# Performance work log

Hardware: AMD Instinct MI355X
Metric: run time of the kernel (lower is better)

The kernel has to match this reference:

```python
import jax, jax.numpy as jnp
import numpy as np

SQRT_2_OVER_PI = 0.79788456

def gelu_tanh(x):
    # tanh-approximate GELU, matches torch F.gelu(approximate='tanh')
    return 0.5 * x * (1.0 + jnp.tanh(SQRT_2_OVER_PI * x * (1.0 + 0.044715 * x * x)))

def gelu_bwd(x):
    # analytical derivative of tanh-approx GELU (same constants as source)
    t = jnp.tanh(SQRT_2_OVER_PI * x * (1.0 + 0.044715 * x * x))
    return 0.5 * x * ((1.0 - t * t) * (SQRT_2_OVER_PI + 0.1070322243 * x * x)) + 0.5 * (1.0 + t)

def setup_inputs() -> dict:
    key = jax.random.key(0)
    ks = jax.random.split(key, 6)
    T, d_phi, d_h = 8192, 4096, 64
    d_mid = 4 * d_h
    return {
        "phi_seq": jax.random.normal(ks[0], (T, d_phi), jnp.float32),
        "C_seq": jax.random.uniform(ks[1], (T,), jnp.float32),
        "theta_K_w": jax.random.normal(ks[2], (d_h, d_phi), jnp.float32) * 0.02,
        "theta_Q_w": jax.random.normal(ks[3], (d_h, d_phi), jnp.float32) * 0.02,
        "W10": jax.random.normal(ks[4], (d_h, d_mid), jnp.float32) * 0.02,
        "b10": jnp.zeros((d_mid,), jnp.float32),
        "W20": jax.random.normal(ks[5], (d_mid,), jnp.float32) * 0.02,
        "b20": jnp.zeros((), jnp.float32),
        "log_eta": jnp.asarray(np.log(0.01), jnp.float32),
    }

def reference(phi_seq, C_seq, theta_K_w, theta_Q_w, W10, b10, W20, b20, log_eta):
    eta = jnp.exp(log_eta)
    # Slow-weight projections hoisted out of the scan (same math, one big GEMM)
    u_Q = phi_seq @ theta_Q_w.T  # [T, d_h]
    u_K = phi_seq @ theta_K_w.T  # [T, d_h]

    def step(carry, inp):
        W1, b1, W2, b2 = carry
        u_q, u_k = inp
        # score with current fast weights
        s = jax.nn.sigmoid(gelu_tanh(u_q @ W1 + b1) @ W2 + b2)
        # update fast weights (inner objective, C_t = 0.0)
        Z1 = u_k @ W1 + b1          # [d_mid]
        X2 = gelu_tanh(Z1)
        pred = jax.nn.sigmoid(X2 @ W2 + b2)
        d_Z2 = 2.0 * pred * pred * (1.0 - pred)  # d/dZ2 of (pred-0)^2
        d_Z1 = (d_Z2 * W2) * gelu_bwd(Z1)
        new_carry = (
            W1 - eta * jnp.outer(u_k, d_Z1),
            b1 - eta * d_Z1,
            W2 - eta * d_Z2 * X2,
            b2 - eta * d_Z2,
        )
        return new_carry, s

    _, scores = jax.lax.scan(step, (W10, b10, W20, b20), (u_Q, u_K))
    outer_loss = jnp.sum((scores - C_seq) ** 2)
    return scores, outer_loss
```

## Files before the change

kernel.cpp:

```cpp
#include <hip/hip_runtime.h>
#include <hip/hip_bf16.h>

#define DH 64
#define DM 256

typedef float f32x2 __attribute__((ext_vector_type(2)));

__device__ __forceinline__ f32x2 sp2(float s) { return (f32x2){s, s}; }
__device__ __forceinline__ f32x2 pkfma(f32x2 a, f32x2 b, f32x2 c) {
#if __has_builtin(__builtin_elementwise_fma)
    return __builtin_elementwise_fma(a, b, c);
#else
    f32x2 r; r.x = fmaf(a.x, b.x, c.x); r.y = fmaf(a.y, b.y, c.y); return r;
#endif
}

__device__ __forceinline__ float tanh_fast(float y) {
    float e = __expf(2.0f * y);
    return 1.0f - 2.0f / (e + 1.0f);
}
__device__ __forceinline__ float sigmoid_fast(float x) {
    return 1.0f / (1.0f + __expf(-x));
}

template <int CTRL, int RMASK>
__device__ __forceinline__ float dpp_term(float x) {
    int p = __builtin_amdgcn_update_dpp(0, __float_as_int(x), CTRL, RMASK, 0xf, false);
    return __int_as_float(p);
}
__device__ __forceinline__ float wave_sum63(float x) {
    x += dpp_term<0xB1,  0xf>(x);
    x += dpp_term<0x4E,  0xf>(x);
    x += dpp_term<0x141, 0xf>(x);
    x += dpp_term<0x140, 0xf>(x);
    x += dpp_term<0x142, 0xa>(x);
    x += dpp_term<0x143, 0xc>(x);
    return x;
}

__global__ __launch_bounds__(256) void proj_kernel(
    const float* __restrict__ phi,
    const float* __restrict__ thK,
    const float* __restrict__ thQ,
    float* __restrict__ u,
    int dphi)
{
    const int tid  = threadIdx.x;
    const int th32 = tid & 31;
    const int tt8  = tid >> 5;
    const int t0   = tt8 * 4;
    const int h0   = th32 * 4;
    const int T0   = blockIdx.x * 32;

    __shared__ float sPhiT[32][36];
    __shared__ float sThT[32][128];

    const int h   = tid >> 1;
    const int ko  = (tid & 1) * 16;
    const float* trow = (h < 64) ? (thQ + (size_t)h * dphi)
                                 : (thK + (size_t)(h - 64) * dphi);
    const int tr  = tid >> 3;
    const int k4p = (tid & 7) * 4;

    float4 pv, tv0, tv1, tv2, tv3;
    pv  = *(const float4*)&phi[(size_t)(T0 + tr) * dphi + k4p];
    tv0 = *(const float4*)&trow[ko + 0];
    tv1 = *(const float4*)&trow[ko + 4];
    tv2 = *(const float4*)&trow[ko + 8];
    tv3 = *(const float4*)&trow[ko + 12];

    float acc[4][4];
    #pragma unroll
    for (int i = 0; i < 4; ++i)
        #pragma unroll
        for (int jj = 0; jj < 4; ++jj) acc[i][jj] = 0.0f;

    const int NC = dphi / 32;
    for (int c = 0; c < NC; ++c) {
        __syncthreads();
        sPhiT[k4p + 0][tr] = pv.x;
        sPhiT[k4p + 1][tr] = pv.y;
        sPhiT[k4p + 2][tr] = pv.z;
        sPhiT[k4p + 3][tr] = pv.w;
        sThT[ko +  0][h] = tv0.x;  sThT[ko +  1][h] = tv0.y;
        sThT[ko +  2][h] = tv0.z;  sThT[ko +  3][h] = tv0.w;
        sThT[ko +  4][h] = tv1.x;  sThT[ko +  5][h] = tv1.y;
        sThT[ko +  6][h] = tv1.z;  sThT[ko +  7][h] = tv1.w;
        sThT[ko +  8][h] = tv2.x;  sThT[ko +  9][h] = tv2.y;
        sThT[ko + 10][h] = tv2.z;  sThT[ko + 11][h] = tv2.w;
        sThT[ko + 12][h] = tv3.x;  sThT[ko + 13][h] = tv3.y;
        sThT[ko + 14][h] = tv3.z;  sThT[ko + 15][h] = tv3.w;
        __syncthreads();
        if (c + 1 < NC) {
            const int kb = (c + 1) * 32;
            pv  = *(const float4*)&phi[(size_t)(T0 + tr) * dphi + kb + k4p];
            tv0 = *(const float4*)&trow[kb + ko + 0];
            tv1 = *(const float4*)&trow[kb + ko + 4];
            tv2 = *(const float4*)&trow[kb + ko + 8];
            tv3 = *(const float4*)&trow[kb + ko + 12];
        }
        #pragma unroll 8
        for (int k = 0; k < 32; ++k) {
            float4 ph = *(const float4*)&sPhiT[k][t0];
            float4 th = *(const float4*)&sThT[k][h0];
            acc[0][0] = fmaf(ph.x, th.x, acc[0][0]);
            acc[0][1] = fmaf(ph.x, th.y, acc[0][1]);
            acc[0][2] = fmaf(ph.x, th.z, acc[0][2]);
            acc[0][3] = fmaf(ph.x, th.w, acc[0][3]);
            acc[1][0] = fmaf(ph.y, th.x, acc[1][0]);
            acc[1][1] = fmaf(ph.y, th.y, acc[1][1]);
            acc[1][2] = fmaf(ph.y, th.z, acc[1][2]);
            acc[1][3] = fmaf(ph.y, th.w, acc[1][3]);
            acc[2][0] = fmaf(ph.z, th.x, acc[2][0]);
            acc[2][1] = fmaf(ph.z, th.y, acc[2][1]);
            acc[2][2] = fmaf(ph.z, th.z, acc[2][2]);
            acc[2][3] = fmaf(ph.z, th.w, acc[2][3]);
            acc[3][0] = fmaf(ph.w, th.x, acc[3][0]);
            acc[3][1] = fmaf(ph.w, th.y, acc[3][1]);
            acc[3][2] = fmaf(ph.w, th.z, acc[3][2]);
            acc[3][3] = fmaf(ph.w, th.w, acc[3][3]);
        }
    }
    #pragma unroll
    for (int i = 0; i < 4; ++i) {
        float4 o;
        o.x = acc[i][0]; o.y = acc[i][1]; o.z = acc[i][2]; o.w = acc[i][3];
        *(float4*)&u[(size_t)(T0 + t0 + i) * 128 + h0] = o;
    }
}

__global__ __launch_bounds__(256) void dots2_kernel(
    const float* __restrict__ u, float2* __restrict__ dd2, int T)
{
    const int t    = (blockIdx.x * 256 + threadIdx.x) >> 6;
    const int lane = threadIdx.x & 63;
    if (t >= T) return;
    float ukt = u[(size_t)t * 128 + 64 + lane];
    float k1 = (t >= 1) ? u[(size_t)(t - 1) * 128 + 64 + lane] : 0.f;
    float k2 = (t >= 2) ? u[(size_t)(t - 2) * 128 + 64 + lane] : 0.f;
    float p1 = k1 * ukt, p2 = k2 * ukt;
    #pragma unroll
    for (int off = 32; off > 0; off >>= 1) {
        p1 += __shfl_xor(p1, off);
        p2 += __shfl_xor(p2, off);
    }
    if (lane == 0) dd2[t] = make_float2(p1, p2);
}

__global__ __launch_bounds__(256, 1) void scan_k4(
    const float* __restrict__ u,
    const float2* __restrict__ dd2g,
    const float* __restrict__ W10,
    const float* __restrict__ b10,
    const float* __restrict__ W20,
    const float* __restrict__ b20,
    const float* __restrict__ log_eta,
    float* __restrict__ e1s,
    float* __restrict__ g2s,
    float* __restrict__ dz2s,
    int T)
{
    const int j    = threadIdx.x;
    const int lane = j & 63;
    const int wv   = j >> 6;
    const int uko  = 16 * wv;

    __shared__ __align__(16) float  ubuf[2][64][68];
    __shared__ __align__(16) float  pbuf[2][4][256];
    __shared__ __align__(16) float  ebufT[4][4][72];
    __shared__ __align__(16) float  pqk[2][4];
    __shared__ __align__(16) float2 dbuf[2][64];

    const int NB = T >> 6;
    const int sl = j >> 2, qq = j & 3;

    {
        const float* src = u + (size_t)sl * 128 + 64 + qq * 16;
        #pragma unroll
        for (int k = 0; k < 4; ++k)
            *(float4*)&ubuf[0][sl][qq * 16 + k * 4] = *(const float4*)&src[k * 4];
        if (j < 64) dbuf[0][j] = dd2g[j];
        if (j < 4)  pqk[1][j] = -2.5e29f;
        float* ez = &ebufT[2][0][0];
        for (int k = j; k < 2 * 4 * 72; k += 256) ez[k] = 0.f;
    }

    f32x2 w1p[32];
    #pragma unroll
    for (int i = 0; i < 16; ++i) {
        float4 wr = *(const float4*)&W10[(uko + i) * DM + lane * 4];
        w1p[2 * i]     = (f32x2){wr.x, wr.y};
        w1p[2 * i + 1] = (f32x2){wr.z, wr.w};
    }
    float b1j = b10[j];
    float w2j = W20[j];
    float b2  = b20[0];
    const float eta = __expf(log_eta[0]);
    float dZ2p = 0.f, en1 = 0.f, en2 = 0.f, x2p = 0.f;

    __syncthreads();

    {
        const float* ur0 = &ubuf[0][0][uko];
        f32x2 a0 = sp2(0.f), a1 = sp2(0.f);
        #pragma unroll
        for (int q = 0; q < 4; ++q) {
            float4 us = *(const float4*)&ur0[q * 4];
            a0 = pkfma(sp2(us.x), w1p[8*q+0], a0); a1 = pkfma(sp2(us.x), w1p[8*q+1], a1);
            a0 = pkfma(sp2(us.y), w1p[8*q+2], a0); a1 = pkfma(sp2(us.y), w1p[8*q+3], a1);
            a0 = pkfma(sp2(us.z), w1p[8*q+4], a0); a1 = pkfma(sp2(us.z), w1p[8*q+5], a1);
            a0 = pkfma(sp2(us.w), w1p[8*q+6], a0); a1 = pkfma(sp2(us.w), w1p[8*q+7], a1);
        }
        float4 wk; wk.x = a0.x; wk.y = a0.y; wk.z = a1.x; wk.w = a1.y;
        *(float4*)&pbuf[0][wv][lane * 4] = wk;
    }
    __syncthreads();

    float4 st[4];
    float2 std2 = make_float2(0.f, 0.f);

    for (int t = 0; t < T; ++t) {
        const int r   = t & 63;
        const int B   = t >> 6;
        const int bs  = B & 1;
        const int pbR = t & 1;

        float4 pqK = *(const float4*)&pqk[pbR ^ 1][0];
        const int sE = (t + 2) & 3;
        float eb0 = ebufT[sE][0][lane];
        float eb1 = ebufT[sE][1][lane];
        float eb2 = ebufT[sE][2][lane];
        float eb3 = ebufT[sE][3][lane];
        float2 dd = dbuf[bs][r];
        float pB0 = pbuf[pbR][0][j], pB1 = pbuf[pbR][1][j];
        float pB2 = pbuf[pbR][2][j], pB3 = pbuf[pbR][3][j];
        const int rn = (t + 1 < T) ? t + 1 : T - 1;
        const int rm = (t >= 2) ? t - 2 : 0;
        const float* urN = &ubuf[(rn >> 6) & 1][rn & 63][uko];
        const float* urM = &ubuf[(rm >> 6) & 1][rm & 63][uko];
        float4 n0 = *(const float4*)&urN[0],  n1 = *(const float4*)&urN[4];
        float4 n2 = *(const float4*)&urN[8],  n3 = *(const float4*)&urN[12];
        float4 m0 = *(const float4*)&urM[0],  m1 = *(const float4*)&urM[4];
        float4 m2 = *(const float4*)&urM[8],  m3 = *(const float4*)&urM[12];

        float zp   = ((pqK.x + pqK.y) + (pqK.z + pqK.w)) + b2;
        float pred = sigmoid_fast(zp);
        float dZ2  = 2.f * pred * pred * (1.f - pred);
        float e1o  = dZ2 * en1;
        if (t > 0) {
            e1s[(size_t)(t - 1) * 256 + j] = e1o;
            g2s[(size_t)(t - 1) * 256 + j] = dZ2 * x2p;
            if (j == 0) dz2s[t - 1] = dZ2;
        }

        f32x2 e1g0 = sp2(dZ2p) * (f32x2){eb0, eb1};
        f32x2 e1g1 = sp2(dZ2p) * (f32x2){eb2, eb3};
        f32x2 a0 = sp2(0.f), a1 = sp2(0.f);
#define ROWK(ib, ums, uns) {                                   \
        f32x2 wa = pkfma(sp2(-(ums)), e1g0, w1p[ib]);          \
        f32x2 wb = pkfma(sp2(-(ums)), e1g1, w1p[(ib) + 1]);    \
        w1p[ib] = wa; w1p[(ib) + 1] = wb;                      \
        a0 = pkfma(sp2(uns), wa, a0);                          \
        a1 = pkfma(sp2(uns), wb, a1); }
        ROWK(0,  m0.x, n0.x); ROWK(2,  m0.y, n0.y);
        ROWK(4,  m0.z, n0.z); ROWK(6,  m0.w, n0.w);
        ROWK(8,  m1.x, n1.x); ROWK(10, m1.y, n1.y);
        ROWK(12, m1.z, n1.z); ROWK(14, m1.w, n1.w);
        ROWK(16, m2.x, n2.x); ROWK(18, m2.y, n2.y);
        ROWK(20, m2.z, n2.z); ROWK(22, m2.w, n2.w);
        ROWK(24, m3.x, n3.x); ROWK(26, m3.y, n3.y);
        ROWK(28, m3.z, n3.z); ROWK(30, m3.w, n3.w);
#undef ROWK
        { float4 wk; wk.x = a0.x; wk.y = a0.y; wk.z = a1.x; wk.w = a1.y;
          *(float4*)&pbuf[pbR ^ 1][wv][lane * 4] = wk; }

        float e1o2 = dZ2p * en2;
        b1j -= e1o;
        w2j  = fmaf(-eta * dZ2, x2p, w2j);
        b2  -= eta * dZ2;
        float Pk = ((pB0 + pB1) + (pB2 + pB3));
        float zk = Pk + b1j - e1o2 * dd.y - e1o * dd.x;
        float tk = tanh_fast(0.79788456f * zk * fmaf(0.044715f, zk * zk, 1.f));
        float x2 = 0.5f * zk * (1.f + tk);
        float gb = 0.5f * zk * ((1.f - tk * tk) *
                   fmaf(0.1070322243f, zk * zk, 0.79788456f))
                 + 0.5f * (1.f + tk);
        float en = eta * w2j * gb;
        ebufT[t & 3][j & 3][j >> 2] = en;
        float pk = wave_sum63(x2 * w2j);
        if (lane == 63) pqk[t & 1][wv] = pk;

        dZ2p = dZ2; en2 = en1; en1 = en; x2p = x2;

        if (r == 0 && B + 1 < NB) {
            const float* src = u + (size_t)((B + 1) * 64 + sl) * 128 + 64 + qq * 16;
            #pragma unroll
            for (int k = 0; k < 4; ++k) st[k] = *(const float4*)&src[k * 4];
            if (j < 64) std2 = dd2g[(B + 1) * 64 + j];
        }
        if (r == 32 && B + 1 < NB) {
            #pragma unroll
            for (int k = 0; k < 4; ++k)
                *(float4*)&ubuf[bs ^ 1][sl][qq * 16 + k * 4] = st[k];
            if (j < 64) dbuf[bs ^ 1][j] = std2;
        }

        asm volatile("s_waitcnt lgkmcnt(0)" ::: "memory");
        __builtin_amdgcn_s_barrier();
        asm volatile("" ::: "memory");
    }

    {
        float4 pqK = *(const float4*)&pqk[(T - 1) & 1][0];
        float zp   = ((pqK.x + pqK.y) + (pqK.z + pqK.w)) + b2;
        float pred = sigmoid_fast(zp);
        float dZ2  = 2.f * pred * pred * (1.f - pred);
        e1s[(size_t)(T - 1) * 256 + j] = dZ2 * en1;
        g2s[(size_t)(T - 1) * 256 + j] = dZ2 * x2p;
        if (j == 0) dz2s[T - 1] = dZ2;
    }
}

#define TB 32
__global__ __launch_bounds__(256) void scores_kernel(
    const float* __restrict__ u,
    const float* __restrict__ e1s,
    const float* __restrict__ g2s,
    const float* __restrict__ dz2s,
    const float* __restrict__ W10,
    const float* __restrict__ b10,
    const float* __restrict__ W20,
    const float* __restrict__ b20,
    const float* __restrict__ log_eta,
    float* __restrict__ out,
    int T)
{
    const int tid = threadIdx.x;
    const int t0  = blockIdx.x * TB;
    const int j   = tid;
    const int wv  = tid >> 6;
    const int lane = tid & 63;

    __shared__ __align__(16) float uq[TB][68];
    __shared__ __align__(16) float uk[TB][68];
    __shared__ __align__(16) float Dl[TB][36];
    __shared__ float redl[2][4];

    #pragma unroll
    for (int k = 0; k < 2; ++k) {
        int idx = tid * 2 + k;
        int tl = idx >> 4, c4 = idx & 15;
        *(float4*)&uq[tl][c4 * 4] = *(const float4*)&u[(size_t)(t0 + tl) * 128 + c4 * 4];
    }
    const float eta = __expf(log_eta[0]);
    float w2p = W20[j];
    float b2p = b20[0];
    float b1j = b10[j];
    __syncthreads();

    float acc[TB];
    {
        float wcol[64];
        #pragma unroll
        for (int i = 0; i < 64; ++i) wcol[i] = W10[i * DM + j];
        for (int tl = 0; tl < TB; ++tl) {
            float a = b1j;
            #pragma unroll
            for (int q = 0; q < 16; ++q) {
                float4 uv = *(const float4*)&uq[tl][q * 4];
                a = fmaf(uv.x, wcol[4*q+0], a);
                a = fmaf(uv.y, wcol[4*q+1], a);
                a = fmaf(uv.z, wcol[4*q+2], a);
                a = fmaf(uv.w, wcol[4*q+3], a);
            }
            acc[tl] = a;
        }
    }

    const int nchunk = t0 / TB + 1;
    for (int c = 0; c < nchunk; ++c) {
        const int sc = c * TB;
        __syncthreads();
        #pragma unroll
        for (int k = 0; k < 2; ++k) {
            int idx = tid * 2 + k;
            int sl = idx >> 4, c4 = idx & 15;
            *(float4*)&uk[sl][c4 * 4] = *(const float4*)&u[(size_t)(sc + sl) * 128 + 64 + c4 * 4];
        }
        __syncthreads();
        {
            int tl = tid & 31, sg = tid >> 5;
            float4 uqr[16];
            #pragma unroll
            for (int q = 0; q < 16; ++q) uqr[q] = *(const float4*)&uq[tl][q * 4];
            #pragma unroll
            for (int k = 0; k < 4; ++k) {
                int sl = sg * 4 + k;
                float d = 0.f;
                #pragma unroll
                for (int q = 0; q < 16; ++q) {
                    float4 ukr = *(const float4*)&uk[sl][q * 4];
                    d = fmaf(ukr.x, uqr[q].x, d);
                    d = fmaf(ukr.y, uqr[q].y, d);
                    d = fmaf(ukr.z, uqr[q].z, d);
                    d = fmaf(ukr.w, uqr[q].w, d);
                }
                Dl[sl][tl] = d;
            }
        }
        __syncthreads();

        const bool lastc = (c == nchunk - 1);
        if (!lastc) {
            float e1acc = 0.f;
            for (int sl = 0; sl < TB; ++sl) {
                const int s = sc + sl;
                float e1v = e1s[(size_t)s * 256 + j];
                float g2v = g2s[(size_t)s * 256 + j];
                float dzv = dz2s[s];
                w2p = fmaf(-eta, g2v, w2p);
                b2p = fmaf(-eta, dzv, b2p);
                e1acc += e1v;
                float4 dreg[8];
                #pragma unroll
                for (int q = 0; q < 8; ++q) dreg[q] = *(const float4*)&Dl[sl][q * 4];
                #pragma unroll
                for (int tl = 0; tl < TB; ++tl) {
                    float D = (tl & 2) ? ((tl & 1) ? dreg[tl>>2].w : dreg[tl>>2].z)
                                       : ((tl & 1) ? dreg[tl>>2].y : dreg[tl>>2].x);
                    acc[tl] = fmaf(-e1v, D, acc[tl]);
                }
            }
            #pragma unroll
            for (int tl = 0; tl < TB; ++tl) acc[tl] -= e1acc;
        } else {
            for (int sl = 0; sl < TB; ++sl) {
                const int s = sc + sl;
                float zq = 0.f;
                #pragma unroll
                for (int tl = 0; tl < TB; ++tl) if (tl == sl) zq = acc[tl];
                float tq = tanh_fast(0.79788456f * zq * fmaf(0.044715f, zq*zq, 1.f));
                float aq = 0.5f * zq * (1.f + tq);
                float v  = wave_sum63(aq * w2p);
                if (lane == 63) redl[sl & 1][wv] = v;
                __syncthreads();
                float zs = redl[sl & 1][0] + redl[sl & 1][1] + redl[sl & 1][2] + redl[sl & 1][3] + b2p;
                if (tid == 0) out[t0 + sl] = sigmoid_fast(zs);

                float e1v = e1s[(size_t)s * 256 + j];
                float g2v = g2s[(size_t)s * 256 + j];
                float dzv = dz2s[s];
                w2p = fmaf(-eta, g2v, w2p);
                b2p = fmaf(-eta, dzv, b2p);
                float4 dreg[8];
                #pragma unroll
                for (int q = 0; q < 8; ++q) dreg[q] = *(const float4*)&Dl[sl][q * 4];
                #pragma unroll
                for (int tl = 0; tl < TB; ++tl) {
                    float D = (tl & 2) ? ((tl & 1) ? dreg[tl>>2].w : dreg[tl>>2].z)
                                       : ((tl & 1) ? dreg[tl>>2].y : dreg[tl>>2].x);
                    float e1m = (tl > sl) ? e1v : 0.f;
                    acc[tl] = fmaf(-e1m, D + 1.f, acc[tl]);
                }
            }
        }
    }
}

__global__ __launch_bounds__(256) void loss_kernel(
    const float* __restrict__ C, float* __restrict__ out, int T)
{
    const int tid = threadIdx.x;
    const int wv = tid >> 6, lane = tid & 63;
    __shared__ float part[4];
    float acc = 0.f;
    for (int t = tid; t < T; t += 256) {
        float d = out[t] - C[t];
        acc = fmaf(d, d, acc);
    }
    acc = wave_sum63(acc);
    if (lane == 63) part[wv] = acc;
    __syncthreads();
    if (tid == 0) out[T] = ((part[0] + part[1]) + (part[2] + part[3]));
}

extern "C" void kernel_launch(void* const* d_in, const int* in_sizes, int n_in,
                              void* d_out, int out_size, void* d_ws, size_t ws_size,
                              hipStream_t stream) {
    const float* phi     = (const float*)d_in[0];
    const float* C_seq   = (const float*)d_in[1];
    const float* thK     = (const float*)d_in[2];
    const float* thQ     = (const float*)d_in[3];
    const float* W10     = (const float*)d_in[4];
    const float* b10     = (const float*)d_in[5];
    const float* W20     = (const float*)d_in[6];
    const float* b20     = (const float*)d_in[7];
    const float* log_eta = (const float*)d_in[8];

    const int T    = in_sizes[1];
    const int dphi = in_sizes[0] / T;

    char* ws = (char*)d_ws;
    float*  uw   = (float*)(ws);
    float2* dd2  = (float2*)(ws + (size_t)T * 128 * 4);
    float*  dz2s = (float*)(ws + (size_t)T * 130 * 4);
    float*  e1s  = (float*)(ws + (size_t)T * 131 * 4);
    float*  g2s  = (float*)(ws + (size_t)T * 387 * 4);

    proj_kernel<<<T / 32, 256, 0, stream>>>(phi, thK, thQ, uw, dphi);
    dots2_kernel<<<T / 4, 256, 0, stream>>>(uw, dd2, T);
    scan_k4<<<1, 256, 0, stream>>>(uw, dd2, W10, b10, W20, b20, log_eta,
                                   e1s, g2s, dz2s, T);
    scores_kernel<<<T / TB, 256, 0, stream>>>(uw, e1s, g2s, dz2s,
                                              W10, b10, W20, b20, log_eta,
                                              (float*)d_out, T);
    loss_kernel<<<1, 256, 0, stream>>>(C_seq, (float*)d_out, T);
}
```

Before: 6.788 ms.

## Replicate per-column nonlinear work in every wave to drop cross-wave LDS exchanges

Each wave now computes the GELU, derivative and score reduction for all 256 mid columns (4 per lane) itself. It no longer has each thread handle one column and exchange the results through the ebufT and pqk shared buffers. This removes one LDS round-trip for the en values and the partial-score gather, and the score is broadcast with a readlane. The cost is four times more transcendental and ALU work per thread on the serial critical path. Global stores of e1s and g2s are vectorized and done only by wave 0.

```diff
diff --git a/kernel.cpp b/kernel.cpp
--- a/kernel.cpp
+++ b/kernel.cpp
@@ -164,11 +164,10 @@
     const int lane = j & 63;
     const int wv   = j >> 6;
     const int uko  = 16 * wv;
+    const int c0   = 4 * lane;
 
     __shared__ __align__(16) float  ubuf[2][64][68];
     __shared__ __align__(16) float  pbuf[2][4][256];
-    __shared__ __align__(16) float  ebufT[4][4][72];
-    __shared__ __align__(16) float  pqk[2][4];
     __shared__ __align__(16) float2 dbuf[2][64];
 
     const int NB = T >> 6;
@@ -180,23 +179,27 @@
         for (int k = 0; k < 4; ++k)
             *(float4*)&ubuf[0][sl][qq * 16 + k * 4] = *(const float4*)&src[k * 4];
         if (j < 64) dbuf[0][j] = dd2g[j];
-        if (j < 4)  pqk[1][j] = -2.5e29f;
-        float* ez = &ebufT[2][0][0];
-        for (int k = j; k < 2 * 4 * 72; k += 256) ez[k] = 0.f;
     }
 
     f32x2 w1p[32];
     #pragma unroll
     for (int i = 0; i < 16; ++i) {
-        float4 wr = *(const float4*)&W10[(uko + i) * DM + lane * 4];
+        float4 wr = *(const float4*)&W10[(uko + i) * DM + c0];
         w1p[2 * i]     = (f32x2){wr.x, wr.y};
         w1p[2 * i + 1] = (f32x2){wr.z, wr.w};
     }
-    float b1j = b10[j];
-    float w2j = W20[j];
+    float4 b14 = *(const float4*)&b10[c0];
+    f32x2 b1v0 = (f32x2){b14.x, b14.y}, b1v1 = (f32x2){b14.z, b14.w};
+    float4 w24 = *(const float4*)&W20[c0];
+    f32x2 w2v0 = (f32x2){w24.x, w24.y}, w2v1 = (f32x2){w24.z, w24.w};
     float b2  = b20[0];
     const float eta = __expf(log_eta[0]);
-    float dZ2p = 0.f, en1 = 0.f, en2 = 0.f, x2p = 0.f;
+
+    float dZ2p = 0.f;
+    f32x2 en1a = sp2(0.f), en1b = sp2(0.f);
+    f32x2 en2a = sp2(0.f), en2b = sp2(0.f);
+    f32x2 x2pa = sp2(0.f), x2pb = sp2(0.f);
+    float zp_prev = -2.5e29f;
 
     __syncthreads();
 
@@ -212,7 +215,7 @@
             a0 = pkfma(sp2(us.w), w1p[8*q+6], a0); a1 = pkfma(sp2(us.w), w1p[8*q+7], a1);
         }
         float4 wk; wk.x = a0.x; wk.y = a0.y; wk.z = a1.x; wk.w = a1.y;
-        *(float4*)&pbuf[0][wv][lane * 4] = wk;
+        *(float4*)&pbuf[0][wv][c0] = wk;
     }
     __syncthreads();
 
@@ -220,20 +223,16 @@
     float2 std2 = make_float2(0.f, 0.f);
 
     for (int t = 0; t < T; ++t) {
-        const int r   = t & 63;
-        const int B   = t >> 6;
-        const int bs  = B & 1;
-        const int pbR = t & 1;
-
-        float4 pqK = *(const float4*)&pqk[pbR ^ 1][0];
-        const int sE = (t + 2) & 3;
-        float eb0 = ebufT[sE][0][lane];
-        float eb1 = ebufT[sE][1][lane];
-        float eb2 = ebufT[sE][2][lane];
-        float eb3 = ebufT[sE][3][lane];
+        const int r  = t & 63;
+        const int B  = t >> 6;
+        const int bs = B & 1;
+        const int pb = t & 1;
+
+        float4 P0 = *(const float4*)&pbuf[pb][0][c0];
+        float4 P1 = *(const float4*)&pbuf[pb][1][c0];
+        float4 P2 = *(const float4*)&pbuf[pb][2][c0];
+        float4 P3 = *(const float4*)&pbuf[pb][3][c0];
         float2 dd = dbuf[bs][r];
-        float pB0 = pbuf[pbR][0][j], pB1 = pbuf[pbR][1][j];
-        float pB2 = pbuf[pbR][2][j], pB3 = pbuf[pbR][3][j];
         const int rn = (t + 1 < T) ? t + 1 : T - 1;
         const int rm = (t >= 2) ? t - 2 : 0;
         const float* urN = &ubuf[(rn >> 6) & 1][rn & 63][uko];
@@ -243,22 +242,29 @@
         float4 m0 = *(const float4*)&urM[0],  m1 = *(const float4*)&urM[4];
         float4 m2 = *(const float4*)&urM[8],  m3 = *(const float4*)&urM[12];
 
-        float zp   = ((pqK.x + pqK.y) + (pqK.z + pqK.w)) + b2;
-        float pred = sigmoid_fast(zp);
+        float pred = sigmoid_fast(zp_prev);
         float dZ2  = 2.f * pred * pred * (1.f - pred);
-        float e1o  = dZ2 * en1;
-        if (t > 0) {
-            e1s[(size_t)(t - 1) * 256 + j] = e1o;
-            g2s[(size_t)(t - 1) * 256 + j] = dZ2 * x2p;
+        f32x2 e1oa  = sp2(dZ2)  * en1a,  e1ob  = sp2(dZ2)  * en1b;
+        f32x2 e1o2a = sp2(dZ2p) * en2a,  e1o2b = sp2(dZ2p) * en2b;
+
+        if (t > 0 && wv == 0) {
+            float4 e1st; e1st.x = e1oa.x; e1st.y = e1oa.y; e1st.z = e1ob.x; e1st.w = e1ob.y;
+            *(float4*)&e1s[(size_t)(t - 1) * 256 + c0] = e1st;
+            f32x2 g2a = sp2(dZ2) * x2pa, g2b = sp2(dZ2) * x2pb;
+            float4 g2st; g2st.x = g2a.x; g2st.y = g2a.y; g2st.z = g2b.x; g2st.w = g2b.y;
+            *(float4*)&g2s[(size_t)(t - 1) * 256 + c0] = g2st;
             if (j == 0) dz2s[t - 1] = dZ2;
         }
 
-        f32x2 e1g0 = sp2(dZ2p) * (f32x2){eb0, eb1};
-        f32x2 e1g1 = sp2(dZ2p) * (f32x2){eb2, eb3};
+        b1v0 = b1v0 - e1oa;  b1v1 = b1v1 - e1ob;
+        w2v0 = pkfma(sp2(-eta * dZ2), x2pa, w2v0);
+        w2v1 = pkfma(sp2(-eta * dZ2), x2pb, w2v1);
+        b2  -= eta * dZ2;
+
         f32x2 a0 = sp2(0.f), a1 = sp2(0.f);
 #define ROWK(ib, ums, uns) {                                   \
-        f32x2 wa = pkfma(sp2(-(ums)), e1g0, w1p[ib]);          \
-        f32x2 wb = pkfma(sp2(-(ums)), e1g1, w1p[(ib) + 1]);    \
+        f32x2 wa = pkfma(sp2(-(ums)), e1o2a, w1p[ib]);         \
+        f32x2 wb = pkfma(sp2(-(ums)), e1o2b, w1p[(ib) + 1]);   \
         w1p[ib] = wa; w1p[(ib) + 1] = wb;                      \
         a0 = pkfma(sp2(uns), wa, a0);                          \
         a1 = pkfma(sp2(uns), wb, a1); }
@@ -272,25 +278,38 @@
         ROWK(28, m3.z, n3.z); ROWK(30, m3.w, n3.w);
 #undef ROWK
         { float4 wk; wk.x = a0.x; wk.y = a0.y; wk.z = a1.x; wk.w = a1.y;
-          *(float4*)&pbuf[pbR ^ 1][wv][lane * 4] = wk; }
-
-        float e1o2 = dZ2p * en2;
-        b1j -= e1o;
-        w2j  = fmaf(-eta * dZ2, x2p, w2j);
-        b2  -= eta * dZ2;
-        float Pk = ((pB0 + pB1) + (pB2 + pB3));
-        float zk = Pk + b1j - e1o2 * dd.y - e1o * dd.x;
-        float tk = tanh_fast(0.79788456f * zk * fmaf(0.044715f, zk * zk, 1.f));
-        float x2 = 0.5f * zk * (1.f + tk);
-        float gb = 0.5f * zk * ((1.f - tk * tk) *
-                   fmaf(0.1070322243f, zk * zk, 0.79788456f))
-                 + 0.5f * (1.f + tk);
-        float en = eta * w2j * gb;
-        ebufT[t & 3][j & 3][j >> 2] = en;
-        float pk = wave_sum63(x2 * w2j);
-        if (lane == 63) pqk[t & 1][wv] = pk;
-
-        dZ2p = dZ2; en2 = en1; en1 = en; x2p = x2;
+          *(float4*)&pbuf[pb ^ 1][wv][c0] = wk; }
+
+        f32x2 zka = (f32x2){(P0.x + P1.x) + (P2.x + P3.x),
+                            (P0.y + P1.y) + (P2.y + P3.y)};
+        f32x2 zkb = (f32x2){(P0.z + P1.z) + (P2.z + P3.z),
+                            (P0.w + P1.w) + (P2.w + P3.w)};
+        zka = zka + b1v0 - sp2(dd.y) * e1o2a - sp2(dd.x) * e1oa;
+        zkb = zkb + b1v1 - sp2(dd.y) * e1o2b - sp2(dd.x) * e1ob;
+
+        float z0 = zka.x, z1 = zka.y, z2 = zkb.x, z3 = zkb.y;
+        float tk0 = tanh_fast(0.79788456f * z0 * fmaf(0.044715f, z0*z0, 1.f));
+        float tk1 = tanh_fast(0.79788456f * z1 * fmaf(0.044715f, z1*z1, 1.f));
+        float tk2 = tanh_fast(0.79788456f * z2 * fmaf(0.044715f, z2*z2, 1.f));
+        float tk3 = tanh_fast(0.79788456f * z3 * fmaf(0.044715f, z3*z3, 1.f));
+        f32x2 x2a = (f32x2){0.5f*z0*(1.f+tk0), 0.5f*z1*(1.f+tk1)};
+        f32x2 x2b = (f32x2){0.5f*z2*(1.f+tk2), 0.5f*z3*(1.f+tk3)};
+        float gb0 = 0.5f*z0*((1.f-tk0*tk0)*fmaf(0.1070322243f, z0*z0, 0.79788456f)) + 0.5f*(1.f+tk0);
+        float gb1 = 0.5f*z1*((1.f-tk1*tk1)*fmaf(0.1070322243f, z1*z1, 0.79788456f)) + 0.5f*(1.f+tk1);
+        float gb2 = 0.5f*z2*((1.f-tk2*tk2)*fmaf(0.1070322243f, z2*z2, 0.79788456f)) + 0.5f*(1.f+tk2);
+        float gb3 = 0.5f*z3*((1.f-tk3*tk3)*fmaf(0.1070322243f, z3*z3, 0.79788456f)) + 0.5f*(1.f+tk3);
+        f32x2 ena = sp2(eta) * w2v0 * (f32x2){gb0, gb1};
+        f32x2 enb = sp2(eta) * w2v1 * (f32x2){gb2, gb3};
+
+        f32x2 pr = x2a * w2v0;
+        pr = pkfma(x2b, w2v1, pr);
+        float red = wave_sum63(pr.x + pr.y);
+        zp_prev = __int_as_float(__builtin_amdgcn_readlane(__float_as_int(red), 63)) + b2;
+
+        dZ2p = dZ2;
+        en2a = en1a; en2b = en1b;
+        en1a = ena;  en1b = enb;
+        x2pa = x2a;  x2pb = x2b;
 
         if (r == 0 && B + 1 < NB) {
             const float* src = u + (size_t)((B + 1) * 64 + sl) * 128 + 64 + qq * 16;
@@ -311,13 +330,17 @@
     }
 
     {
-        float4 pqK = *(const float4*)&pqk[(T - 1) & 1][0];
-        float zp   = ((pqK.x + pqK.y) + (pqK.z + pqK.w)) + b2;
-        float pred = sigmoid_fast(zp);
+        float pred = sigmoid_fast(zp_prev);
         float dZ2  = 2.f * pred * pred * (1.f - pred);
-        e1s[(size_t)(T - 1) * 256 + j] = dZ2 * en1;
-        g2s[(size_t)(T - 1) * 256 + j] = dZ2 * x2p;
-        if (j == 0) dz2s[T - 1] = dZ2;
+        if (wv == 0) {
+            f32x2 e1a = sp2(dZ2) * en1a, e1b = sp2(dZ2) * en1b;
+            float4 e1st; e1st.x = e1a.x; e1st.y = e1a.y; e1st.z = e1b.x; e1st.w = e1b.y;
+            *(float4*)&e1s[(size_t)(T - 1) * 256 + c0] = e1st;
+            f32x2 g2a = sp2(dZ2) * x2pa, g2b = sp2(dZ2) * x2pb;
+            float4 g2st; g2st.x = g2a.x; g2st.y = g2a.y; g2st.z = g2b.x; g2st.w = g2b.y;
+            *(float4*)&g2s[(size_t)(T - 1) * 256 + c0] = g2st;
+            if (j == 0) dz2s[T - 1] = dZ2;
+        }
     }
 }
 
```

New measurement: 7.527 ms. 10.9% more time.

## Checkpoint fast-weight snapshots every 128 steps to shorten score recomputation

Applied to the files above, without the earlier changes.

The sequential scan kernel now writes snapshots of W1, b1, W2 and b2 to workspace every 128 timesteps. The scores kernel starts from the nearest snapshot instead of the initial weights, so it replays only the rank-1 updates since that checkpoint rather than all prior steps. This removes the quadratic-in-T replay work in the scores kernel. The cost is extra global stores inside the latency-critical single-block scan and more workspace, and the snapshot timing (t&127==1 for W, ==0 for biases) must line up exactly with the update ordering.

```diff
diff --git a/kernel.cpp b/kernel.cpp
--- a/kernel.cpp
+++ b/kernel.cpp
@@ -158,6 +158,10 @@
     float* __restrict__ e1s,
     float* __restrict__ g2s,
     float* __restrict__ dz2s,
+    float* __restrict__ snapW,
+    float* __restrict__ snapB1,
+    float* __restrict__ snapW2,
+    float* __restrict__ snapB2,
     int T)
 {
     const int j    = threadIdx.x;
@@ -274,10 +278,29 @@
         { float4 wk; wk.x = a0.x; wk.y = a0.y; wk.z = a1.x; wk.w = a1.y;
           *(float4*)&pbuf[pbR ^ 1][wv][lane * 4] = wk; }
 
+        if ((t & 127) == 1) {
+            float* dW = snapW + (size_t)(t >> 7) * 16384;
+            #pragma unroll
+            for (int i = 0; i < 16; ++i) {
+                float4 wr;
+                wr.x = w1p[2 * i].x;     wr.y = w1p[2 * i].y;
+                wr.z = w1p[2 * i + 1].x; wr.w = w1p[2 * i + 1].y;
+                *(float4*)&dW[(uko + i) * 256 + lane * 4] = wr;
+            }
+        }
+
         float e1o2 = dZ2p * en2;
         b1j -= e1o;
         w2j  = fmaf(-eta * dZ2, x2p, w2j);
         b2  -= eta * dZ2;
+
+        if ((t & 127) == 0) {
+            const int cs_ = t >> 7;
+            snapB1[cs_ * 256 + j] = b1j;
+            snapW2[cs_ * 256 + j] = w2j;
+            if (j == 0) snapB2[cs_] = b2;
+        }
+
         float Pk = ((pB0 + pB1) + (pB2 + pB3));
         float zk = Pk + b1j - e1o2 * dd.y - e1o * dd.x;
         float tk = tanh_fast(0.79788456f * zk * fmaf(0.044715f, zk * zk, 1.f));
@@ -327,10 +350,10 @@
     const float* __restrict__ e1s,
     const float* __restrict__ g2s,
     const float* __restrict__ dz2s,
-    const float* __restrict__ W10,
-    const float* __restrict__ b10,
-    const float* __restrict__ W20,
-    const float* __restrict__ b20,
+    const float* __restrict__ snapW,
+    const float* __restrict__ snapB1,
+    const float* __restrict__ snapW2,
+    const float* __restrict__ snapB2,
     const float* __restrict__ log_eta,
     float* __restrict__ out,
     int T)
@@ -340,6 +363,7 @@
     const int j   = tid;
     const int wv  = tid >> 6;
     const int lane = tid & 63;
+    const int snapc = t0 >> 7;
 
     __shared__ __align__(16) float uq[TB][68];
     __shared__ __align__(16) float uk[TB][68];
@@ -353,16 +377,17 @@
         *(float4*)&uq[tl][c4 * 4] = *(const float4*)&u[(size_t)(t0 + tl) * 128 + c4 * 4];
     }
     const float eta = __expf(log_eta[0]);
-    float w2p = W20[j];
-    float b2p = b20[0];
-    float b1j = b10[j];
+    float w2p = snapW2[snapc * 256 + j];
+    float b2p = snapB2[snapc];
+    float b1j = snapB1[snapc * 256 + j];
     __syncthreads();
 
     float acc[TB];
     {
+        const float* Wsn = snapW + (size_t)snapc * 16384;
         float wcol[64];
         #pragma unroll
-        for (int i = 0; i < 64; ++i) wcol[i] = W10[i * DM + j];
+        for (int i = 0; i < 64; ++i) wcol[i] = Wsn[i * DM + j];
         for (int tl = 0; tl < TB; ++tl) {
             float a = b1j;
             #pragma unroll
@@ -377,8 +402,9 @@
         }
     }
 
-    const int nchunk = t0 / TB + 1;
-    for (int c = 0; c < nchunk; ++c) {
+    const int cs = snapc << 2;
+    const int ce = t0 >> 5;
+    for (int c = cs; c <= ce; ++c) {
         const int sc = c * TB;
         __syncthreads();
         #pragma unroll
@@ -410,7 +436,7 @@
         }
         __syncthreads();
 
-        const bool lastc = (c == nchunk - 1);
+        const bool lastc = (c == ce);
         if (!lastc) {
             float e1acc = 0.f;
             for (int sl = 0; sl < TB; ++sl) {
@@ -499,20 +525,27 @@
 
     const int T    = in_sizes[1];
     const int dphi = in_sizes[0] / T;
+    const int NS   = T >> 7;
 
     char* ws = (char*)d_ws;
-    float*  uw   = (float*)(ws);
-    float2* dd2  = (float2*)(ws + (size_t)T * 128 * 4);
-    float*  dz2s = (float*)(ws + (size_t)T * 130 * 4);
-    float*  e1s  = (float*)(ws + (size_t)T * 131 * 4);
-    float*  g2s  = (float*)(ws + (size_t)T * 387 * 4);
+    size_t off = 0;
+    float*  uw     = (float*)(ws + off);  off += (size_t)T * 128 * 4;
+    float2* dd2    = (float2*)(ws + off); off += (size_t)T * 2 * 4;
+    float*  dz2s   = (float*)(ws + off);  off += (size_t)T * 4;
+    float*  e1s    = (float*)(ws + off);  off += (size_t)T * 256 * 4;
+    float*  g2s    = (float*)(ws + off);  off += (size_t)T * 256 * 4;
+    float*  snapW  = (float*)(ws + off);  off += (size_t)NS * 16384 * 4;
+    float*  snapB1 = (float*)(ws + off);  off += (size_t)NS * 256 * 4;
+    float*  snapW2 = (float*)(ws + off);  off += (size_t)NS * 256 * 4;
+    float*  snapB2 = (float*)(ws + off);  off += (size_t)NS * 4;
 
     proj_kernel<<<T / 32, 256, 0, stream>>>(phi, thK, thQ, uw, dphi);
     dots2_kernel<<<T / 4, 256, 0, stream>>>(uw, dd2, T);
     scan_k4<<<1, 256, 0, stream>>>(uw, dd2, W10, b10, W20, b20, log_eta,
-                                   e1s, g2s, dz2s, T);
+                                   e1s, g2s, dz2s,
+                                   snapW, snapB1, snapW2, snapB2, T);
     scores_kernel<<<T / TB, 256, 0, stream>>>(uw, e1s, g2s, dz2s,
-                                              W10, b10, W20, b20, log_eta,
-                                              (float*)d_out, T);
+                                              snapW, snapB1, snapW2, snapB2,
+                                              log_eta, (float*)d_out, T);
     loss_kernel<<<1, 256, 0, stream>>>(C_seq, (float*)d_out, T);
 }
```

Result: faster. 5.808 ms (-14.4%).
